# Optimization experiments

Measured on AMD Instinct MI355X. Metric: run time of the kernel, lower is better.

The kernel has to match this reference:

```python
import jax, jax.numpy as jnp
import numpy as np

B, L, D, H, HD = 4, 4096, 512, 8, 64
BS = 64                 # block_size
NB = L // BS            # num blocks (== max_num_blocks)
MAXNB = 64


def setup_inputs() -> dict:
    key = jax.random.key(0)
    ks = jax.random.split(key, 11)
    s_in = 1.0 / np.sqrt(D)
    s_hd = 1.0 / np.sqrt(HD)
    s_o = 1.0 / np.sqrt(H * HD)
    return {
        "inputs_q": jax.random.normal(ks[0], (B, L, D), jnp.float32),
        "Wq": jax.random.normal(ks[1], (D, H, HD), jnp.float32) * s_in,
        "bq": jnp.zeros((H, HD), jnp.float32),
        "Wk": jax.random.normal(ks[2], (D, H, HD), jnp.float32) * s_in,
        "bk": jnp.zeros((H, HD), jnp.float32),
        "Wv": jax.random.normal(ks[3], (D, H, HD), jnp.float32) * s_in,
        "bv": jnp.zeros((H, HD), jnp.float32),
        "Wsort": jax.random.normal(ks[4], (HD, MAXNB), jnp.float32) * s_hd,
        "bsort": jnp.zeros((MAXNB,), jnp.float32),
        "Wout": jax.random.normal(ks[5], (H, HD, D), jnp.float32) * s_o,
        "bout": jnp.zeros((D,), jnp.float32),
    }


def _block_attention(q, k, v):
    # q,k,v: [b, n_blocks, block, heads, head_dim]; attention within each block
    scale = 1.0 / np.sqrt(HD)
    scores = jnp.einsum("bnqhd,bnkhd->bnhqk", q, k) * scale
    w = jax.nn.softmax(scores, axis=-1)
    return jnp.einsum("bnhqk,bnkhd->bnqhd", w, v)


def reference(inputs_q, Wq, bq, Wk, bk, Wv, bv, Wsort, bsort, Wout, bout):
    # self-attention: inputs_kv = inputs_q; seq_len == blocks_total_len so no padding
    q = jnp.einsum("bld,dhk->blhk", inputs_q, Wq) + bq
    k = jnp.einsum("bld,dhk->blhk", inputs_q, Wk) + bk
    v = jnp.einsum("bld,dhk->blhk", inputs_q, Wv) + bv

    block_q = q.reshape(B, NB, BS, H, HD)
    block_k = k.reshape(B, NB, BS, H, HD)
    block_v = v.reshape(B, NB, BS, H, HD)

    # non-causal: sum keys within each block -> [b, n_kv, h, hd]
    sum_key = jnp.sum(block_k, axis=2)
    sort_out = jnp.einsum("bnhk,ko->bnho", sum_key, Wsort) + bsort
    sort_out = sort_out[:, :, :, :NB]
    permutation = jax.nn.softmax(sort_out, axis=-1)  # [b, n_kv, h, n_q]

    # faithful to original einsum subscripts ('k' and 'l' both contracted)
    sorted_key = jnp.einsum("bkshd,bnhl->bnshd", block_k, permutation)
    sorted_value = jnp.einsum("bkshd,bnhl->bnshd", block_v, permutation)

    x = _block_attention(block_q, block_k, block_v)
    x = x + _block_attention(block_q, sorted_key, sorted_value)

    x = x.reshape(B, L, H, HD)
    out = jnp.einsum("blhd,hdf->blf", x, Wout) + bout
    return out
```

## Files before the change

kernel.cpp:

```cpp
#include <hip/hip_runtime.h>


constexpr int BB   = 4;
constexpr int LL   = 4096;
constexpr int DD   = 512;
constexpr int HH   = 8;
constexpr int HDIM = 64;
constexpr int BS   = 64;
constexpr int NBLK = 64;
constexpr int MTOT = BB * LL;

using f32x4  = __attribute__((ext_vector_type(4))) float;
typedef __attribute__((ext_vector_type(8))) __bf16 bf16x8;

static __device__ __forceinline__ ushort f2bf(float f) {
  uint u = __float_as_uint(f);
  uint r = (u + 0x7fffu + ((u >> 16) & 1u)) >> 16;
  return (ushort)r;
}
static __device__ __forceinline__ float bf2f(ushort u) { return __uint_as_float((uint)u << 16); }
static __device__ __forceinline__ float bflo(uint u) { return __uint_as_float(u << 16); }
static __device__ __forceinline__ float bfhi(uint u) { return __uint_as_float(u & 0xffff0000u); }

static __device__ __forceinline__ int swb(int row, int cb) {
  return (row << 6) + ((cb ^ ((row & 7) << 4)) >> 1);
}

#define GLOBAL_AS(p) ((const __attribute__((address_space(1))) void*)(p))
#define LDS_AS(p)    ((__attribute__((address_space(3))) void*)(p))
#define SB0()        __builtin_amdgcn_sched_barrier(0)

__global__ __launch_bounds__(256) void f32_to_bf16_vec(
    const float* __restrict__ src, ushort* __restrict__ dst)
{
  const int i = blockIdx.x * 256 + threadIdx.x;
  float4 v = reinterpret_cast<const float4*>(src)[i];
  ushort4 o;
  o.x = f2bf(v.x); o.y = f2bf(v.y); o.z = f2bf(v.z); o.w = f2bf(v.w);
  reinterpret_cast<ushort4*>(dst)[i] = o;
}

__global__ __launch_bounds__(256) void transpose_cast4(
    const float* __restrict__ Wq, const float* __restrict__ Wk,
    const float* __restrict__ Wv, const float* __restrict__ Wo,
    ushort* __restrict__ Wqkv_t, ushort* __restrict__ Wout_t)
{
  __shared__ float tile[32][33];
  const int z  = blockIdx.z;
  const float* src = (z == 0) ? Wq : (z == 1) ? Wk : (z == 2) ? Wv : Wo;
  ushort* dst = (z < 3) ? (Wqkv_t + (size_t)z * 512 * 512) : Wout_t;
  const int tx = threadIdx.x & 31, ty = threadIdx.x >> 5;
  const int r0 = blockIdx.y * 32, c0 = blockIdx.x * 32;
  #pragma unroll
  for (int q = 0; q < 4; ++q)
    tile[ty + 8 * q][tx] = src[(size_t)(r0 + ty + 8 * q) * 512 + c0 + tx];
  __syncthreads();
  #pragma unroll
  for (int q = 0; q < 4; ++q)
    dst[(size_t)(c0 + ty + 8 * q) * 512 + r0 + tx] = f2bf(tile[tx][ty + 8 * q]);
}

__global__ void concat_bias(const float* __restrict__ bq, const float* __restrict__ bk,
                            const float* __restrict__ bv, float* __restrict__ o)
{
  const int t = threadIdx.x;
  o[t] = bq[t]; o[512 + t] = bk[t]; o[1024 + t] = bv[t];
}

template<int MODE>
__global__ __launch_bounds__(256, 3) void gemm_pipe3(
    const ushort* __restrict__ A, const ushort* __restrict__ Bt,
    const float* __restrict__ bias,
    ushort* __restrict__ Cq, ushort* __restrict__ Ck, ushort* __restrict__ Cv,
    float* __restrict__ Cf, int N, int NBX)
{
  constexpr int K  = 512;
  constexpr int NT = K / 32;
  __shared__ __align__(16) ushort sA[3][128 * 32];
  __shared__ __align__(16) ushort sB[3][128 * 32];

  const int tid  = threadIdx.x;
  const int lane = tid & 63;
  const int w    = tid >> 6;
  const int wr   = w >> 1, wc = w & 1;
  const int lr   = lane & 15;
  const int kq   = lane >> 4;

  const int nwg  = NBX * 128;
  const int cpx  = nwg >> 3;
  const int swz  = ((int)blockIdx.x & 7) * cpx + ((int)blockIdx.x >> 3);
  const int nb   = swz % NBX;
  const int mb   = swz / NBX;
  const int brow = mb * 128;
  const int bcol = nb * 128;

  auto stageA = [&](int buf, int t, int j) {
    const int c   = j * 256 + tid;
    const int row = c >> 2, ch = c & 3;
    const ushort* src = A + (size_t)(brow + row) * K + t * 32 + ((ch ^ (row & 3)) << 3);
    __builtin_amdgcn_global_load_lds(GLOBAL_AS(src),
        LDS_AS(&sA[buf][(j * 256 + (w << 6)) << 3]), 16, 0, 0);
  };
  auto stageB = [&](int buf, int t, int j) {
    const int c   = j * 256 + tid;
    const int row = c >> 2, ch = c & 3;
    const ushort* src = Bt + (size_t)(bcol + row) * K + t * 32 + ((ch ^ (row & 3)) << 3);
    __builtin_amdgcn_global_load_lds(GLOBAL_AS(src),
        LDS_AS(&sB[buf][(j * 256 + (w << 6)) << 3]), 16, 0, 0);
  };
  auto ldA = [&](int buf, int mf) -> bf16x8 {
    const int row = (wr << 6) + (mf << 4) + lr;
    return *reinterpret_cast<const bf16x8*>(&sA[buf][(row << 5) + ((kq ^ (row & 3)) << 3)]);
  };
  auto ldB = [&](int buf, int nf) -> bf16x8 {
    const int row = (wc << 6) + (nf << 4) + lr;
    return *reinterpret_cast<const bf16x8*>(&sB[buf][(row << 5) + ((kq ^ (row & 3)) << 3)]);
  };

  f32x4 acc[4][4];
  #pragma unroll
  for (int mi = 0; mi < 4; ++mi)
    #pragma unroll
    for (int ni = 0; ni < 4; ++ni)
      acc[mi][ni] = (f32x4){0.f, 0.f, 0.f, 0.f};

  stageA(0, 0, 0); stageA(0, 0, 1); stageB(0, 0, 0); stageB(0, 0, 1);
  stageA(1, 1, 0); stageA(1, 1, 1); stageB(1, 1, 0); stageB(1, 1, 1);
  asm volatile("s_waitcnt vmcnt(4)" ::: "memory");
  SB0(); __builtin_amdgcn_s_barrier(); SB0();

  for (int t = 0; t < NT; ++t) {
    const int buf  = t % 3;
    const int nbuf = (t + 2) % 3;
    const bool more = (t + 2) < NT;

    bf16x8 af[4], bfr[4];
    #pragma unroll
    for (int mf = 0; mf < 4; ++mf) af[mf] = ldA(buf, mf);
    #pragma unroll
    for (int nf = 0; nf < 4; ++nf) bfr[nf] = ldB(buf, nf);
    if (more) { stageA(nbuf, t + 2, 0); stageA(nbuf, t + 2, 1);
                stageB(nbuf, t + 2, 0); stageB(nbuf, t + 2, 1); }
    SB0();
    __builtin_amdgcn_s_setprio(1);
    #pragma unroll
    for (int mi = 0; mi < 4; ++mi)
      #pragma unroll
      for (int ni = 0; ni < 4; ++ni)
        acc[mi][ni] = __builtin_amdgcn_mfma_f32_16x16x32_bf16(af[mi], bfr[ni], acc[mi][ni], 0, 0, 0);
    __builtin_amdgcn_s_setprio(0);
    SB0();
    if (more) asm volatile("s_waitcnt vmcnt(4)" ::: "memory");
    else      asm volatile("s_waitcnt vmcnt(0)" ::: "memory");
    SB0(); __builtin_amdgcn_s_barrier(); SB0();
  }

  #pragma unroll
  for (int mi = 0; mi < 4; ++mi) {
    #pragma unroll
    for (int ni = 0; ni < 4; ++ni) {
      const int col = bcol + wc * 64 + ni * 16 + lr;
      const float bb = bias[col];
      if (MODE == 0) {
        const int which = col >> 9;
        const int nn    = col & 511;
        ushort* dst = (which == 0) ? Cq : ((which == 1) ? Ck : Cv);
        #pragma unroll
        for (int r = 0; r < 4; ++r) {
          const int row = brow + wr * 64 + mi * 16 + kq * 4 + r;
          dst[(size_t)row * DD + nn] = f2bf(acc[mi][ni][r] + bb);
        }
      } else {
        #pragma unroll
        for (int r = 0; r < 4; ++r) {
          const int row = brow + wr * 64 + mi * 16 + kq * 4 + r;
          Cf[(size_t)row * N + col] = acc[mi][ni][r] + bb;
        }
      }
    }
  }
}

__global__ __launch_bounds__(256) void sumkv_fused(
    const ushort* __restrict__ K, const ushort* __restrict__ V,
    ushort* __restrict__ Khi, ushort* __restrict__ Klo, ushort* __restrict__ Vb)
{
  __shared__ float kbuf[4][64][9];
  __shared__ float vbuf[4][64][9];
  const int bs   = blockIdx.x;
  const int b    = bs >> 6, s = bs & 63;
  const int lane = threadIdx.x & 63;
  const int kbq  = threadIdx.x >> 6;
  const size_t rowbase = ((size_t)b * LL + s) * DD + lane * 8;

  float ak[8] = {0,0,0,0,0,0,0,0}, av[8] = {0,0,0,0,0,0,0,0};
  #pragma unroll
  for (int i = 0; i < 16; ++i) {
    const size_t off = rowbase + (size_t)(kbq * 16 + i) * BS * DD;
    uint4 ku = *reinterpret_cast<const uint4*>(K + off);
    uint4 vu = *reinterpret_cast<const uint4*>(V + off);
    ak[0] += bflo(ku.x); ak[1] += bfhi(ku.x); ak[2] += bflo(ku.y); ak[3] += bfhi(ku.y);
    ak[4] += bflo(ku.z); ak[5] += bfhi(ku.z); ak[6] += bflo(ku.w); ak[7] += bfhi(ku.w);
    av[0] += bflo(vu.x); av[1] += bfhi(vu.x); av[2] += bflo(vu.y); av[3] += bfhi(vu.y);
    av[4] += bflo(vu.z); av[5] += bfhi(vu.z); av[6] += bflo(vu.w); av[7] += bfhi(vu.w);
  }
  #pragma unroll
  for (int j = 0; j < 8; ++j) { kbuf[kbq][lane][j] = ak[j]; vbuf[kbq][lane][j] = av[j]; }
  __syncthreads();

  const size_t wbase = (size_t)bs * DD + lane * 8;
  if (kbq == 0) {
    uint4 hi4, lo4;
    uint* hp = reinterpret_cast<uint*>(&hi4);
    uint* lp = reinterpret_cast<uint*>(&lo4);
    #pragma unroll
    for (int p = 0; p < 4; ++p) {
      uint hw = 0, lw = 0;
      #pragma unroll
      for (int q = 0; q < 2; ++q) {
        const int j = p * 2 + q;
        const float t = kbuf[0][lane][j] + kbuf[1][lane][j] +
                        kbuf[2][lane][j] + kbuf[3][lane][j];
        const ushort h = f2bf(t);
        const ushort l = f2bf(t - bf2f(h));
        hw |= (uint)h << (16 * q);
        lw |= (uint)l << (16 * q);
      }
      hp[p] = hw; lp[p] = lw;
    }
    *reinterpret_cast<uint4*>(Khi + wbase) = hi4;
    *reinterpret_cast<uint4*>(Klo + wbase) = lo4;
  } else if (kbq == 1) {
    uint4 o4;
    uint* op = reinterpret_cast<uint*>(&o4);
    #pragma unroll
    for (int p = 0; p < 4; ++p) {
      uint wv = 0;
      #pragma unroll
      for (int q = 0; q < 2; ++q) {
        const int j = p * 2 + q;
        const float t = vbuf[0][lane][j] + vbuf[1][lane][j] +
                        vbuf[2][lane][j] + vbuf[3][lane][j];
        wv |= (uint)f2bf(t) << (16 * q);
      }
      op[p] = wv;
    }
    *reinterpret_cast<uint4*>(Vb + wbase) = o4;
  }
}

__global__ __launch_bounds__(256) void attn_mfma(
    const ushort* __restrict__ Q, const ushort* __restrict__ Kg,
    const ushort* __restrict__ Vg, const ushort* __restrict__ Khi,
    const ushort* __restrict__ Klo, const ushort* __restrict__ Vsb,
    ushort* __restrict__ X)
{
  __shared__ __align__(16) ushort sA[64 * 64];
  __shared__ __align__(16) ushort sC[64 * 64];
  __shared__ __align__(16) ushort sVt[64 * 64];
  __shared__ __align__(16) ushort sP[64 * 64];
  const int n = blockIdx.x, h = blockIdx.y, b = blockIdx.z;
  const int tid  = threadIdx.x;
  const int lane = tid & 63;
  const int w    = tid >> 6;
  const int lr   = lane & 15, hi4 = lane >> 4;
  const float scale = 0.125f;

  const size_t tbase = ((size_t)(b * LL + n * BS)) * DD + h * HDIM;
  const size_t sbase = ((size_t)(b * BS)) * DD + h * HDIM;

  uint4 k1[2], v1[2], k2h[2], k2l[2], v2[2];
  int rr[2], cc[2];
  #pragma unroll
  for (int it = 0; it < 2; ++it) {
    const int i  = tid + it * 256;
    const int r  = i >> 3;
    const int c8 = (i & 7) << 3;
    rr[it] = r; cc[it] = c8;
    const size_t g1 = tbase + (size_t)r * DD + c8;
    const size_t g2 = sbase + (size_t)r * DD + c8;
    k1[it]  = *reinterpret_cast<const uint4*>(Kg  + g1);
    v1[it]  = *reinterpret_cast<const uint4*>(Vg  + g1);
    k2h[it] = *reinterpret_cast<const uint4*>(Khi + g2);
    k2l[it] = *reinterpret_cast<const uint4*>(Klo + g2);
    v2[it]  = *reinterpret_cast<const uint4*>(Vsb + g2);
  }
  bf16x8 qf[2];
  #pragma unroll
  for (int ks = 0; ks < 2; ++ks)
    qf[ks] = *reinterpret_cast<const bf16x8*>(
        Q + tbase + (size_t)(w * 16 + lr) * DD + ks * 32 + hi4 * 8);

  #pragma unroll
  for (int it = 0; it < 2; ++it) {
    *reinterpret_cast<uint4*>(&sA[swb(rr[it], cc[it] << 1)]) = k1[it];
    const uint u[4] = {v1[it].x, v1[it].y, v1[it].z, v1[it].w};
    #pragma unroll
    for (int j = 0; j < 4; ++j) {
      sVt[swb(cc[it] + 2 * j,     rr[it] << 1)] = (ushort)(u[j] & 0xffff);
      sVt[swb(cc[it] + 2 * j + 1, rr[it] << 1)] = (ushort)(u[j] >> 16);
    }
  }
  __syncthreads();

  f32x4 xacc[4];
  #pragma unroll
  for (int dt = 0; dt < 4; ++dt) xacc[dt] = (f32x4){0.f, 0.f, 0.f, 0.f};

  {
    f32x4 st[4];
    #pragma unroll
    for (int t = 0; t < 4; ++t) st[t] = (f32x4){0.f, 0.f, 0.f, 0.f};
    #pragma unroll
    for (int ks = 0; ks < 2; ++ks) {
      #pragma unroll
      for (int t = 0; t < 4; ++t) {
        bf16x8 kf = *reinterpret_cast<const bf16x8*>(
            &sA[swb(t * 16 + lr, (ks * 32 + hi4 * 8) << 1)]);
        st[t] = __builtin_amdgcn_mfma_f32_16x16x32_bf16(kf, qf[ks], st[t], 0, 0, 0);
      }
    }
    float e[4][4];
    float mx = -1e30f;
    #pragma unroll
    for (int t = 0; t < 4; ++t)
      #pragma unroll
      for (int r = 0; r < 4; ++r) { e[t][r] = st[t][r] * scale; mx = fmaxf(mx, e[t][r]); }
    mx = fmaxf(mx, __shfl_xor(mx, 16));
    mx = fmaxf(mx, __shfl_xor(mx, 32));
    float sum = 0.f;
    #pragma unroll
    for (int t = 0; t < 4; ++t)
      #pragma unroll
      for (int r = 0; r < 4; ++r) { e[t][r] = __expf(e[t][r] - mx); sum += e[t][r]; }
    sum += __shfl_xor(sum, 16);
    sum += __shfl_xor(sum, 32);
    const float inv = 1.0f / sum;
    #pragma unroll
    for (int t = 0; t < 4; ++t) {
      ushort4 p4;
      p4.x = f2bf(e[t][0] * inv); p4.y = f2bf(e[t][1] * inv);
      p4.z = f2bf(e[t][2] * inv); p4.w = f2bf(e[t][3] * inv);
      *reinterpret_cast<ushort4*>(&sP[swb(w * 16 + lr, (t * 16 + hi4 * 4) << 1)]) = p4;
    }
    #pragma unroll
    for (int ks = 0; ks < 2; ++ks) {
      bf16x8 pa = *reinterpret_cast<const bf16x8*>(
          &sP[swb(w * 16 + lr, (ks * 32 + hi4 * 8) << 1)]);
      #pragma unroll
      for (int dt = 0; dt < 4; ++dt) {
        bf16x8 vb = *reinterpret_cast<const bf16x8*>(
            &sVt[swb(dt * 16 + lr, (ks * 32 + hi4 * 8) << 1)]);
        xacc[dt] = __builtin_amdgcn_mfma_f32_16x16x32_bf16(pa, vb, xacc[dt], 0, 0, 0);
      }
    }
  }
  __syncthreads();

  #pragma unroll
  for (int it = 0; it < 2; ++it) {
    *reinterpret_cast<uint4*>(&sA[swb(rr[it], cc[it] << 1)]) = k2h[it];
    *reinterpret_cast<uint4*>(&sC[swb(rr[it], cc[it] << 1)]) = k2l[it];
    const uint u[4] = {v2[it].x, v2[it].y, v2[it].z, v2[it].w};
    #pragma unroll
    for (int j = 0; j < 4; ++j) {
      sVt[swb(cc[it] + 2 * j,     rr[it] << 1)] = (ushort)(u[j] & 0xffff);
      sVt[swb(cc[it] + 2 * j + 1, rr[it] << 1)] = (ushort)(u[j] >> 16);
    }
  }
  __syncthreads();

  {
    f32x4 st[4];
    #pragma unroll
    for (int t = 0; t < 4; ++t) st[t] = (f32x4){0.f, 0.f, 0.f, 0.f};
    #pragma unroll
    for (int ks = 0; ks < 2; ++ks) {
      #pragma unroll
      for (int t = 0; t < 4; ++t) {
        bf16x8 kh = *reinterpret_cast<const bf16x8*>(
            &sA[swb(t * 16 + lr, (ks * 32 + hi4 * 8) << 1)]);
        st[t] = __builtin_amdgcn_mfma_f32_16x16x32_bf16(kh, qf[ks], st[t], 0, 0, 0);
        bf16x8 kl = *reinterpret_cast<const bf16x8*>(
            &sC[swb(t * 16 + lr, (ks * 32 + hi4 * 8) << 1)]);
        st[t] = __builtin_amdgcn_mfma_f32_16x16x32_bf16(kl, qf[ks], st[t], 0, 0, 0);
      }
    }
    float e[4][4];
    float mx = -1e30f;
    #pragma unroll
    for (int t = 0; t < 4; ++t)
      #pragma unroll
      for (int r = 0; r < 4; ++r) { e[t][r] = st[t][r] * scale; mx = fmaxf(mx, e[t][r]); }
    mx = fmaxf(mx, __shfl_xor(mx, 16));
    mx = fmaxf(mx, __shfl_xor(mx, 32));
    float sum = 0.f;
    #pragma unroll
    for (int t = 0; t < 4; ++t)
      #pragma unroll
      for (int r = 0; r < 4; ++r) { e[t][r] = __expf(e[t][r] - mx); sum += e[t][r]; }
    sum += __shfl_xor(sum, 16);
    sum += __shfl_xor(sum, 32);
    const float inv = 1.0f / sum;
    #pragma unroll
    for (int t = 0; t < 4; ++t) {
      ushort4 p4;
      p4.x = f2bf(e[t][0] * inv); p4.y = f2bf(e[t][1] * inv);
      p4.z = f2bf(e[t][2] * inv); p4.w = f2bf(e[t][3] * inv);
      *reinterpret_cast<ushort4*>(&sP[swb(w * 16 + lr, (t * 16 + hi4 * 4) << 1)]) = p4;
    }
    #pragma unroll
    for (int ks = 0; ks < 2; ++ks) {
      bf16x8 pa = *reinterpret_cast<const bf16x8*>(
          &sP[swb(w * 16 + lr, (ks * 32 + hi4 * 8) << 1)]);
      #pragma unroll
      for (int dt = 0; dt < 4; ++dt) {
        bf16x8 vb = *reinterpret_cast<const bf16x8*>(
            &sVt[swb(dt * 16 + lr, (ks * 32 + hi4 * 8) << 1)]);
        xacc[dt] = __builtin_amdgcn_mfma_f32_16x16x32_bf16(pa, vb, xacc[dt], 0, 0, 0);
      }
    }
  }

  #pragma unroll
  for (int dt = 0; dt < 4; ++dt)
    #pragma unroll
    for (int r = 0; r < 4; ++r)
      X[tbase + (size_t)(w * 16 + hi4 * 4 + r) * DD + dt * 16 + lr] = f2bf(xacc[dt][r]);
}

extern "C" void kernel_launch(void* const* d_in, const int* in_sizes, int n_in,
                              void* d_out, int out_size, void* d_ws, size_t ws_size,
                              hipStream_t stream) {
  const float* x_in = (const float*)d_in[0];
  const float* Wq   = (const float*)d_in[1];
  const float* bq   = (const float*)d_in[2];
  const float* Wk   = (const float*)d_in[3];
  const float* bk   = (const float*)d_in[4];
  const float* Wv   = (const float*)d_in[5];
  const float* bv   = (const float*)d_in[6];
  const float* Wout = (const float*)d_in[9];
  const float* bout = (const float*)d_in[10];
  float* out = (float*)d_out;

  const size_t NTOK = (size_t)MTOT * DD;
  const size_t NSUM = (size_t)BB * BS * DD;
  char* ws = (char*)d_ws;
  ushort* xb      = (ushort*)ws;            ws += NTOK * 2;
  ushort* Qb      = (ushort*)ws;            ws += NTOK * 2;
  ushort* Kb      = (ushort*)ws;            ws += NTOK * 2;
  ushort* Vb      = (ushort*)ws;            ws += NTOK * 2;
  ushort* Xb      = (ushort*)ws;            ws += NTOK * 2;
  ushort* Wqkv_t  = (ushort*)ws;            ws += (size_t)1536 * 512 * 2;
  ushort* Wout_t  = (ushort*)ws;            ws += (size_t)512 * 512 * 2;
  float*  bias_qkv= (float*)ws;             ws += 2048 * 4;
  ushort* KhiB    = (ushort*)ws;            ws += NSUM * 2;
  ushort* KloB    = (ushort*)ws;            ws += NSUM * 2;
  ushort* VsB     = (ushort*)ws;            ws += NSUM * 2;

  f32_to_bf16_vec<<<NTOK / 4 / 256, 256, 0, stream>>>(x_in, xb);
  transpose_cast4<<<dim3(16, 16, 4), 256, 0, stream>>>(
      Wq, Wk, Wv, Wout, Wqkv_t, Wout_t);
  concat_bias<<<1, 512, 0, stream>>>(bq, bk, bv, bias_qkv);

  gemm_pipe3<0><<<12 * 128, 256, 0, stream>>>(
      xb, Wqkv_t, bias_qkv, Qb, Kb, Vb, nullptr, 1536, 12);

  sumkv_fused<<<BB * BS, 256, 0, stream>>>(Kb, Vb, KhiB, KloB, VsB);

  attn_mfma<<<dim3(NBLK, HH, BB), 256, 0, stream>>>(Qb, Kb, Vb, KhiB, KloB, VsB, Xb);

  gemm_pipe3<1><<<4 * 128, 256, 0, stream>>>(
      Xb, Wout_t, bout, nullptr, nullptr, nullptr, out, 512, 4);
}
```

Measured before the change: 101.6 us.

## Replace QKV GEMM with 256x256-tile 8-phase pipelined kernel, retune output GEMM

The QKV projection GEMM moves from 128x128 tiles with a triple-buffered 32-wide K loop to a 512-thread kernel with 256x256 tiles, 64-wide K steps, double buffering and an 8-phase schedule. Each phase interleaves global-to-LDS staging with MFMA bursts, which cuts global traffic per FLOP and overlaps loads with compute. The output-projection GEMM becomes a dedicated kernel with a different LDS XOR swizzle and a launch-bounds occupancy hint of 2 instead of 3. Costs: far more accumulator registers, 384 workgroups (fewer than the 256 CUs can balance evenly), and many barriers per K step.

```diff
diff --git a/kernel.cpp b/kernel.cpp
--- a/kernel.cpp
+++ b/kernel.cpp
@@ -67,15 +67,183 @@
   o[t] = bq[t]; o[512 + t] = bk[t]; o[1024 + t] = bv[t];
 }
 
-template<int MODE>
-__global__ __launch_bounds__(256, 3) void gemm_pipe3(
+#define MFMA8(MF0)                                                              \
+    __builtin_amdgcn_s_setprio(1);                                              \
+    _Pragma("unroll")                                                           \
+    for (int nf = 0; nf < 4; ++nf) {                                            \
+      acc[MF0][nf]     = __builtin_amdgcn_mfma_f32_16x16x32_bf16(a00, br[nf][0], acc[MF0][nf], 0, 0, 0);     \
+      acc[MF0][nf]     = __builtin_amdgcn_mfma_f32_16x16x32_bf16(a01, br[nf][1], acc[MF0][nf], 0, 0, 0);     \
+      acc[MF0 + 1][nf] = __builtin_amdgcn_mfma_f32_16x16x32_bf16(a10, br[nf][0], acc[MF0 + 1][nf], 0, 0, 0); \
+      acc[MF0 + 1][nf] = __builtin_amdgcn_mfma_f32_16x16x32_bf16(a11, br[nf][1], acc[MF0 + 1][nf], 0, 0, 0); \
+    }                                                                           \
+    __builtin_amdgcn_s_setprio(0);
+
+#define RDAQ(BASE, MF0)                                                         \
+    bf16x8 a00 = rdA(BASE, MF0, 0), a01 = rdA(BASE, MF0, 1);                    \
+    bf16x8 a10 = rdA(BASE, MF0 + 1, 0), a11 = rdA(BASE, MF0 + 1, 1);
+
+#define BAR() SB0(); __builtin_amdgcn_s_barrier(); SB0()
+
+__global__ __launch_bounds__(512, 2) void gemm_8phase(
     const ushort* __restrict__ A, const ushort* __restrict__ Bt,
     const float* __restrict__ bias,
-    ushort* __restrict__ Cq, ushort* __restrict__ Ck, ushort* __restrict__ Cv,
-    float* __restrict__ Cf, int N, int NBX)
+    ushort* __restrict__ Cq, ushort* __restrict__ Ck, ushort* __restrict__ Cv)
+{
+  constexpr int K = 512;
+  __shared__ __align__(16) ushort sA[2][256 * 64];
+  __shared__ __align__(16) ushort sB[2][256 * 64];
+
+  const int tid  = threadIdx.x;
+  const int lane = tid & 63;
+  const int w    = tid >> 6;
+  const int wr   = w >> 2;
+  const int wc   = w & 3;
+  const int lr   = lane & 15;
+  const int kq   = lane >> 4;
+
+  const int cpx  = 384 >> 3;
+  const int swz  = ((int)blockIdx.x & 7) * cpx + ((int)blockIdx.x >> 3);
+  const int nb   = swz % 6;
+  const int mb   = swz / 6;
+  const int brow = mb * 256;
+  const int bcol = nb * 256;
+
+  auto stA = [&](int buf, int kt, int half, int j) {
+    const int c = j * 512 + tid;
+    const int row = c >> 3, g = c & 7;
+    const ushort* src = A + (size_t)(brow + half * 128 + row) * K + kt * 64 + ((g ^ (row & 7)) << 3);
+    __builtin_amdgcn_global_load_lds(GLOBAL_AS(src),
+        LDS_AS(&sA[buf][(half * 1024 + j * 512 + w * 64) * 8]), 16, 0, 0);
+  };
+  auto stB = [&](int buf, int kt, int half, int j) {
+    const int c = j * 512 + tid;
+    const int row = c >> 3, g = c & 7;
+    const ushort* src = Bt + (size_t)(bcol + half * 128 + row) * K + kt * 64 + ((g ^ (row & 7)) << 3);
+    __builtin_amdgcn_global_load_lds(GLOBAL_AS(src),
+        LDS_AS(&sB[buf][(half * 1024 + j * 512 + w * 64) * 8]), 16, 0, 0);
+  };
+  auto rdA = [&](const ushort* base, int mf, int ks) -> bf16x8 {
+    const int row = (wr << 7) + (mf << 4) + lr;
+    return *reinterpret_cast<const bf16x8*>(
+        &base[(row << 6) + ((((ks << 2) + kq) ^ (row & 7)) << 3)]);
+  };
+  auto rdB = [&](const ushort* base, int nf, int ks) -> bf16x8 {
+    const int row = (wc << 6) + (nf << 4) + lr;
+    return *reinterpret_cast<const bf16x8*>(
+        &base[(row << 6) + ((((ks << 2) + kq) ^ (row & 7)) << 3)]);
+  };
+
+  f32x4 acc[8][4];
+  #pragma unroll
+  for (int mf = 0; mf < 8; ++mf)
+    #pragma unroll
+    for (int nf = 0; nf < 4; ++nf)
+      acc[mf][nf] = (f32x4){0.f, 0.f, 0.f, 0.f};
+
+  stA(0, 0, 0, 0); stA(0, 0, 0, 1); stA(0, 0, 1, 0); stA(0, 0, 1, 1);
+  stB(0, 0, 0, 0); stB(0, 0, 0, 1); stB(0, 0, 1, 0); stB(0, 0, 1, 1);
+  stB(1, 1, 0, 0); stB(1, 1, 0, 1); stB(1, 1, 1, 0); stB(1, 1, 1, 1);
+  asm volatile("s_waitcnt vmcnt(4)" ::: "memory");
+  BAR();
+
+  for (int i = 0; i < 4; ++i) {
+    const int t1 = 2 * i + 1, t2 = 2 * i + 2, t3 = 2 * i + 3;
+    const bool h2 = t2 < 8, h3 = t3 < 8;
+    bf16x8 br[4][2];
+
+    {
+      #pragma unroll
+      for (int nf = 0; nf < 4; ++nf) { br[nf][0] = rdB(sB[0], nf, 0); br[nf][1] = rdB(sB[0], nf, 1); }
+      RDAQ(sA[0], 0);
+      stA(1, t1, 0, 0); stA(1, t1, 0, 1);
+      BAR();
+      MFMA8(0);
+      BAR();
+    }
+    {
+      RDAQ(sA[0], 2);
+      stA(1, t1, 1, 0); stA(1, t1, 1, 1);
+      if (h2) { stB(0, t2, 0, 0); stB(0, t2, 0, 1); }
+      BAR();
+      MFMA8(2);
+      BAR();
+    }
+    {
+      RDAQ(sA[0], 4);
+      if (h2) { stB(0, t2, 1, 0); stB(0, t2, 1, 1); }
+      BAR();
+      MFMA8(4);
+      BAR();
+    }
+    {
+      RDAQ(sA[0], 6);
+      BAR();
+      MFMA8(6);
+      SB0();
+      if (h2) asm volatile("s_waitcnt vmcnt(4)" ::: "memory");
+      else    asm volatile("s_waitcnt vmcnt(0)" ::: "memory");
+      BAR();
+    }
+    {
+      #pragma unroll
+      for (int nf = 0; nf < 4; ++nf) { br[nf][0] = rdB(sB[1], nf, 0); br[nf][1] = rdB(sB[1], nf, 1); }
+      RDAQ(sA[1], 0);
+      if (h2) { stA(0, t2, 0, 0); stA(0, t2, 0, 1); }
+      BAR();
+      MFMA8(0);
+      BAR();
+    }
+    {
+      RDAQ(sA[1], 2);
+      if (h2) { stA(0, t2, 1, 0); stA(0, t2, 1, 1); }
+      if (h3) { stB(1, t3, 0, 0); stB(1, t3, 0, 1); }
+      BAR();
+      MFMA8(2);
+      BAR();
+    }
+    {
+      RDAQ(sA[1], 4);
+      if (h3) { stB(1, t3, 1, 0); stB(1, t3, 1, 1); }
+      BAR();
+      MFMA8(4);
+      BAR();
+    }
+    {
+      RDAQ(sA[1], 6);
+      BAR();
+      MFMA8(6);
+      SB0();
+      if (h3) asm volatile("s_waitcnt vmcnt(4)" ::: "memory");
+      else    asm volatile("s_waitcnt vmcnt(0)" ::: "memory");
+      BAR();
+    }
+  }
+
+  #pragma unroll
+  for (int mf = 0; mf < 8; ++mf) {
+    #pragma unroll
+    for (int nf = 0; nf < 4; ++nf) {
+      const int col = bcol + wc * 64 + nf * 16 + lr;
+      const float bb = bias[col];
+      const int which = col >> 9;
+      const int nn    = col & 511;
+      ushort* dst = (which == 0) ? Cq : ((which == 1) ? Ck : Cv);
+      #pragma unroll
+      for (int r = 0; r < 4; ++r) {
+        const int row = brow + wr * 128 + mf * 16 + kq * 4 + r;
+        dst[(size_t)row * DD + nn] = f2bf(acc[mf][nf][r] + bb);
+      }
+    }
+  }
+}
+
+__global__ __launch_bounds__(256, 2) void gemm_out(
+    const ushort* __restrict__ A, const ushort* __restrict__ Bt,
+    const float* __restrict__ bias, float* __restrict__ Cf)
 {
   constexpr int K  = 512;
   constexpr int NT = K / 32;
+  constexpr int N  = 512;
   __shared__ __align__(16) ushort sA[3][128 * 32];
   __shared__ __align__(16) ushort sB[3][128 * 32];
 
@@ -86,35 +254,34 @@
   const int lr   = lane & 15;
   const int kq   = lane >> 4;
 
-  const int nwg  = NBX * 128;
-  const int cpx  = nwg >> 3;
+  const int cpx  = 512 >> 3;
   const int swz  = ((int)blockIdx.x & 7) * cpx + ((int)blockIdx.x >> 3);
-  const int nb   = swz % NBX;
-  const int mb   = swz / NBX;
+  const int nb   = swz % 4;
+  const int mb   = swz / 4;
   const int brow = mb * 128;
   const int bcol = nb * 128;
 
   auto stageA = [&](int buf, int t, int j) {
     const int c   = j * 256 + tid;
     const int row = c >> 2, ch = c & 3;
-    const ushort* src = A + (size_t)(brow + row) * K + t * 32 + ((ch ^ (row & 3)) << 3);
+    const ushort* src = A + (size_t)(brow + row) * K + t * 32 + ((ch ^ ((row >> 1) & 3)) << 3);
     __builtin_amdgcn_global_load_lds(GLOBAL_AS(src),
         LDS_AS(&sA[buf][(j * 256 + (w << 6)) << 3]), 16, 0, 0);
   };
   auto stageB = [&](int buf, int t, int j) {
     const int c   = j * 256 + tid;
     const int row = c >> 2, ch = c & 3;
-    const ushort* src = Bt + (size_t)(bcol + row) * K + t * 32 + ((ch ^ (row & 3)) << 3);
+    const ushort* src = Bt + (size_t)(bcol + row) * K + t * 32 + ((ch ^ ((row >> 1) & 3)) << 3);
     __builtin_amdgcn_global_load_lds(GLOBAL_AS(src),
         LDS_AS(&sB[buf][(j * 256 + (w << 6)) << 3]), 16, 0, 0);
   };
   auto ldA = [&](int buf, int mf) -> bf16x8 {
     const int row = (wr << 6) + (mf << 4) + lr;
-    return *reinterpret_cast<const bf16x8*>(&sA[buf][(row << 5) + ((kq ^ (row & 3)) << 3)]);
+    return *reinterpret_cast<const bf16x8*>(&sA[buf][(row << 5) + ((kq ^ ((row >> 1) & 3)) << 3)]);
   };
   auto ldB = [&](int buf, int nf) -> bf16x8 {
     const int row = (wc << 6) + (nf << 4) + lr;
-    return *reinterpret_cast<const bf16x8*>(&sB[buf][(row << 5) + ((kq ^ (row & 3)) << 3)]);
+    return *reinterpret_cast<const bf16x8*>(&sB[buf][(row << 5) + ((kq ^ ((row >> 1) & 3)) << 3)]);
   };
 
   f32x4 acc[4][4];
@@ -161,21 +328,10 @@
     for (int ni = 0; ni < 4; ++ni) {
       const int col = bcol + wc * 64 + ni * 16 + lr;
       const float bb = bias[col];
-      if (MODE == 0) {
-        const int which = col >> 9;
-        const int nn    = col & 511;
-        ushort* dst = (which == 0) ? Cq : ((which == 1) ? Ck : Cv);
-        #pragma unroll
-        for (int r = 0; r < 4; ++r) {
-          const int row = brow + wr * 64 + mi * 16 + kq * 4 + r;
-          dst[(size_t)row * DD + nn] = f2bf(acc[mi][ni][r] + bb);
-        }
-      } else {
-        #pragma unroll
-        for (int r = 0; r < 4; ++r) {
-          const int row = brow + wr * 64 + mi * 16 + kq * 4 + r;
-          Cf[(size_t)row * N + col] = acc[mi][ni][r] + bb;
-        }
+      #pragma unroll
+      for (int r = 0; r < 4; ++r) {
+        const int row = brow + wr * 64 + mi * 16 + kq * 4 + r;
+        Cf[(size_t)row * N + col] = acc[mi][ni][r] + bb;
       }
     }
   }
@@ -463,13 +619,11 @@
       Wq, Wk, Wv, Wout, Wqkv_t, Wout_t);
   concat_bias<<<1, 512, 0, stream>>>(bq, bk, bv, bias_qkv);
 
-  gemm_pipe3<0><<<12 * 128, 256, 0, stream>>>(
-      xb, Wqkv_t, bias_qkv, Qb, Kb, Vb, nullptr, 1536, 12);
+  gemm_8phase<<<384, 512, 0, stream>>>(xb, Wqkv_t, bias_qkv, Qb, Kb, Vb);
 
   sumkv_fused<<<BB * BS, 256, 0, stream>>>(Kb, Vb, KhiB, KloB, VsB);
 
   attn_mfma<<<dim3(NBLK, HH, BB), 256, 0, stream>>>(Qb, Kb, Vb, KhiB, KloB, VsB, Xb);
 
-  gemm_pipe3<1><<<4 * 128, 256, 0, stream>>>(
-      Xb, Wout_t, bout, nullptr, nullptr, nullptr, out, 512, 4);
-}
+  gemm_out<<<512, 256, 0, stream>>>(Xb, Wout_t, bout, out);
+}
```

Result: slower. 104.4 us (+2.7%).
